# Performance work log

Hardware: AMD Instinct MI355X
Metric: run time of the kernel (lower is better)

## Reference

```python
import jax, jax.numpy as jnp
import numpy as np

B, N, E = 4, 2048, 512
H = 8
HD = E // H  # 64
SCALE = HD ** -0.5


def setup_inputs() -> dict:
    key = jax.random.key(0)
    k1, k2, k3 = jax.random.split(key, 3)
    x = jax.random.normal(k1, (B, N, E), dtype=jnp.float32)
    # xavier-uniform-like scaling for weights
    w_qkv = jax.random.normal(k2, (3 * E, E), dtype=jnp.float32) * (2.0 / (4 * E)) ** 0.5
    b_qkv = jnp.zeros((3 * E,), dtype=jnp.float32)
    w_out = jax.random.normal(k3, (E, E), dtype=jnp.float32) * (1.0 / E) ** 0.5
    b_out = jnp.zeros((E,), dtype=jnp.float32)
    return {"x": x, "w_qkv": w_qkv, "b_qkv": b_qkv, "w_out": w_out, "b_out": b_out}


def reference(x, w_qkv, b_qkv, w_out, b_out):
    b_sz, n_patches, _ = x.shape
    # qkv projection: [B,N,3E] -> [B,N,3,H,HD] -> [B,H,3,N,HD]
    qkv = (jnp.einsum('bne,fe->bnf', x, w_qkv) + b_qkv)
    qkv = qkv.reshape(b_sz, n_patches, 3, H, HD).transpose(0, 3, 2, 1, 4)
    q, k, v = qkv[:, :, 0], qkv[:, :, 1], qkv[:, :, 2]  # each [B,H,N,HD]
    attn = jnp.einsum('bhqd,bhkd->bhqk', q * SCALE, k)  # [B,H,N,N]
    attn = jax.nn.softmax(attn, axis=-1)
    # attn_dropout p=0.0 -> identity in reference
    out = jnp.einsum('bhqk,bhkd->bhqd', attn, v)  # [B,H,N,HD]
    out = out.transpose(0, 2, 1, 3).reshape(b_sz, n_patches, E)
    out = jnp.einsum('bne,fe->bnf', out, w_out) + b_out
    return out
```

## Files before the change

kernel.cpp:

```cpp
#include <hip/hip_runtime.h>

#define BB   4
#define SEQ  2048
#define EMB  512
#define NH   8
#define HD   64
#define QSCALE 0.18033688011f

typedef __bf16 bf16x8 __attribute__((ext_vector_type(8)));
typedef float  f32x4  __attribute__((ext_vector_type(4)));

__device__ __forceinline__ short f2bf(float f) {
  union { float f; unsigned u; } v; v.f = f;
  unsigned r = v.u + 0x7fffu + ((v.u >> 16) & 1u);
  return (short)(r >> 16);
}

__device__ __forceinline__ unsigned pk_bf16(float a, float b) {
#if __has_builtin(__builtin_amdgcn_cvt_pk_bf16_f32)
  typedef __bf16 bf16v2 __attribute__((ext_vector_type(2)));
  union { bf16v2 v; unsigned u; } cv;
  cv.v = __builtin_amdgcn_cvt_pk_bf16_f32(a, b);
  return cv.u;
#else
  return (unsigned)(unsigned short)f2bf(a) | ((unsigned)(unsigned short)f2bf(b) << 16);
#endif
}

__device__ __forceinline__ float fexp2(float x) {
#if __has_builtin(__builtin_amdgcn_exp2f)
  return __builtin_amdgcn_exp2f(x);
#else
  return exp2f(x);
#endif
}

__device__ __forceinline__ void gl_lds16(const void* g, void* l) {
  __builtin_amdgcn_global_load_lds(
      (const __attribute__((address_space(1))) unsigned int*)g,
      (__attribute__((address_space(3))) unsigned int*)l, 16, 0, 0);
}

__global__ __launch_bounds__(256) void cast_all(const float* __restrict__ x,
                                                const float* __restrict__ wq,
                                                const float* __restrict__ wo,
                                                short* __restrict__ xb,
                                                short* __restrict__ wqb,
                                                short* __restrict__ wob) {
  int i = blockIdx.x * 256 + threadIdx.x;
  const float* src; short* dst; int off;
  if (i < 1048576)      { src = x;  dst = xb;  off = i; }
  else if (i < 1245184) { src = wq; dst = wqb; off = i - 1048576; }
  else                  { src = wo; dst = wob; off = i - 1245184; }
  float4 v = ((const float4*)src)[off];
  uint2 o; o.x = pk_bf16(v.x, v.y); o.y = pk_bf16(v.z, v.w);
  *(uint2*)&dst[off * 4] = o;
}

__global__ __launch_bounds__(256) void qkv_gemm(const short* __restrict__ A,
                                                const short* __restrict__ W,
                                                const float* __restrict__ bias,
                                                short* __restrict__ qo,
                                                short* __restrict__ ko,
                                                short* __restrict__ vto) {
  __shared__ __align__(16) short As[128 * 64];
  __shared__ __align__(16) short Bs[128 * 64];
  const int tid  = threadIdx.x;
  const int lane = tid & 63, wave = tid >> 6;
  const int wm = wave >> 1, wf = wave & 1;
  const int col = lane & 15, quad = lane >> 4;
  const int m0 = blockIdx.x * 128, f0 = blockIdx.y * 128;

  const short* aSrc[4]; const short* wSrc[4];
#pragma unroll
  for (int rd = 0; rd < 4; ++rd) {
    int slot = rd * 256 + tid;
    int row = slot >> 3;
    int cb  = (slot & 7) ^ (row & 7);
    aSrc[rd] = A + (size_t)(m0 + row) * 512 + cb * 8;
    wSrc[rd] = W + (size_t)(f0 + row) * 512 + cb * 8;
  }
  int aOff[2][4], bOff[2][4];
#pragma unroll
  for (int kk = 0; kk < 2; ++kk)
#pragma unroll
    for (int i = 0; i < 4; ++i) {
      aOff[kk][i] = (wm * 64 + i * 16 + col) * 64 + (((kk * 4 + quad) ^ (col & 7)) * 8);
      bOff[kk][i] = (wf * 64 + i * 16 + col) * 64 + (((kk * 4 + quad) ^ (col & 7)) * 8);
    }

  f32x4 acc[4][4];
#pragma unroll
  for (int i = 0; i < 4; ++i)
#pragma unroll
    for (int j = 0; j < 4; ++j)
#pragma unroll
      for (int r = 0; r < 4; ++r) acc[i][j][r] = 0.f;

  for (int kt = 0; kt < 8; ++kt) {
    __syncthreads();
#pragma unroll
    for (int rd = 0; rd < 4; ++rd) {
      gl_lds16(aSrc[rd], (char*)As + rd * 4096 + wave * 1024);
      gl_lds16(wSrc[rd], (char*)Bs + rd * 4096 + wave * 1024);
      aSrc[rd] += 64; wSrc[rd] += 64;
    }
    __syncthreads();
#pragma unroll
    for (int kk = 0; kk < 2; ++kk) {
      bf16x8 af[4], bw[4];
#pragma unroll
      for (int i = 0; i < 4; ++i) af[i] = *(const bf16x8*)&As[aOff[kk][i]];
#pragma unroll
      for (int j = 0; j < 4; ++j) bw[j] = *(const bf16x8*)&Bs[bOff[kk][j]];
#pragma unroll
      for (int i = 0; i < 4; ++i)
#pragma unroll
        for (int j = 0; j < 4; ++j)
          acc[i][j] = __builtin_amdgcn_mfma_f32_16x16x32_bf16(af[i], bw[j], acc[i][j], 0, 0, 0);
    }
  }

#pragma unroll
  for (int j = 0; j < 4; ++j) {
    const int f = f0 + wf * 64 + j * 16 + col;
    const float bv = bias[f];
    const int sIdx = f >> 9;
    const int h = (f >> 6) & 7;
    const int d = f & 63;
#pragma unroll
    for (int i = 0; i < 4; ++i) {
      const int mbase = m0 + wm * 64 + i * 16 + quad * 4;
      const int b = mbase >> 11;
      const int n = mbase & 2047;
      const size_t bh = (size_t)(b * NH + h);
      if (sIdx == 2) {
        uint2 pk;
        pk.x = pk_bf16(acc[i][j][0] + bv, acc[i][j][1] + bv);
        pk.y = pk_bf16(acc[i][j][2] + bv, acc[i][j][3] + bv);
        *(uint2*)&vto[(bh * HD + d) * SEQ + n] = pk;
      } else if (sIdx == 0) {
#pragma unroll
        for (int r = 0; r < 4; ++r)
          qo[(bh * SEQ + n + r) * HD + d] = f2bf((acc[i][j][r] + bv) * QSCALE);
      } else {
#pragma unroll
        for (int r = 0; r < 4; ++r)
          ko[(bh * SEQ + n + r) * HD + d] = f2bf(acc[i][j][r] + bv);
      }
    }
  }
}

__global__ __launch_bounds__(256) void attn_kernel(const short* __restrict__ q,
                                                   const short* __restrict__ k,
                                                   const short* __restrict__ vt,
                                                   short* __restrict__ o) {
  __shared__ __align__(16) short Ks[64 * 64];
  __shared__ __align__(16) short Vs[64 * 64];
  __shared__ __align__(16) short Ps[4 * 32 * 72];
  __shared__ float Ls[4 * 32];
  const int tid  = threadIdx.x;
  const int lane = tid & 63, wave = tid >> 6;
  const int col = lane & 15, quad = lane >> 4;
  const int bh = blockIdx.x & 31;
  const int q0 = (blockIdx.x >> 5) * 128;
  const size_t bhBase = (size_t)bh * SEQ * HD;

  bf16x8 qf[2][2];
#pragma unroll
  for (int t = 0; t < 2; ++t)
#pragma unroll
    for (int ks = 0; ks < 2; ++ks)
      qf[t][ks] = *(const bf16x8*)&q[bhBase +
          (size_t)(q0 + wave * 32 + t * 16 + col) * HD + ks * 32 + quad * 8];

  const int rowL = tid >> 3,         cbL = (tid & 7) ^ (rowL & 7);
  const int rowH = (256 + tid) >> 3, cbH = (tid & 7) ^ (rowH & 7);
  const short* ksrcL = k  + bhBase + (size_t)rowL * HD + cbL * 8;
  const short* ksrcH = k  + bhBase + (size_t)rowH * HD + cbH * 8;
  const short* vsrcL = vt + bhBase + (size_t)rowL * SEQ + cbL * 8;
  const short* vsrcH = vt + bhBase + (size_t)rowH * SEQ + cbH * 8;
  char* ldsKL = (char*)Ks + wave * 1024;
  char* ldsKH = (char*)Ks + 4096 + wave * 1024;
  char* ldsVL = (char*)Vs + wave * 1024;
  char* ldsVH = (char*)Vs + 4096 + wave * 1024;

  const int wbase = wave * 32 * 72;
  int kfO[4][2], vfO[2][4], pwO[4][2], prO[2][2];
#pragma unroll
  for (int kt = 0; kt < 4; ++kt)
#pragma unroll
    for (int ks = 0; ks < 2; ++ks)
      kfO[kt][ks] = (kt * 16 + col) * 64 + (((ks * 4 + quad) ^ (col & 7)) * 8);
#pragma unroll
  for (int ks2 = 0; ks2 < 2; ++ks2)
#pragma unroll
    for (int nt = 0; nt < 4; ++nt)
      vfO[ks2][nt] = (nt * 16 + col) * 64 + (((ks2 * 4 + quad) ^ (col & 7)) * 8);
#pragma unroll
  for (int kt = 0; kt < 4; ++kt)
#pragma unroll
    for (int t = 0; t < 2; ++t)
      pwO[kt][t] = wbase + (t * 16 + col) * 72 + kt * 16 + quad * 4;
#pragma unroll
  for (int t = 0; t < 2; ++t)
#pragma unroll
    for (int ks2 = 0; ks2 < 2; ++ks2)
      prO[t][ks2] = wbase + (t * 16 + col) * 72 + ks2 * 32 + quad * 8;

  f32x4 oacc[2][4];
#pragma unroll
  for (int t = 0; t < 2; ++t)
#pragma unroll
    for (int nt = 0; nt < 4; ++nt)
#pragma unroll
      for (int r = 0; r < 4; ++r) oacc[t][nt][r] = 0.f;
  float lpart[2] = {0.f, 0.f};

  for (int n0 = 0; n0 < SEQ; n0 += 64) {
    __syncthreads();
    gl_lds16(ksrcL, ldsKL);
    gl_lds16(ksrcH, ldsKH);
    gl_lds16(vsrcL, ldsVL);
    gl_lds16(vsrcH, ldsVH);
    ksrcL += 64 * HD; ksrcH += 64 * HD; vsrcL += 64; vsrcH += 64;
    __syncthreads();

    f32x4 sacc[4][2];
#pragma unroll
    for (int kt = 0; kt < 4; ++kt)
#pragma unroll
      for (int t = 0; t < 2; ++t)
#pragma unroll
        for (int r = 0; r < 4; ++r) sacc[kt][t][r] = 0.f;
#pragma unroll
    for (int kt = 0; kt < 4; ++kt)
#pragma unroll
      for (int ks = 0; ks < 2; ++ks) {
        bf16x8 kf = *(const bf16x8*)&Ks[kfO[kt][ks]];
#pragma unroll
        for (int t = 0; t < 2; ++t)
          sacc[kt][t] = __builtin_amdgcn_mfma_f32_16x16x32_bf16(kf, qf[t][ks], sacc[kt][t], 0, 0, 0);
      }

#pragma unroll
    for (int kt = 0; kt < 4; ++kt)
#pragma unroll
      for (int t = 0; t < 2; ++t) {
        float p0 = fexp2(sacc[kt][t][0]);
        float p1 = fexp2(sacc[kt][t][1]);
        float p2 = fexp2(sacc[kt][t][2]);
        float p3 = fexp2(sacc[kt][t][3]);
        lpart[t] += (p0 + p1) + (p2 + p3);
        uint2 w; w.x = pk_bf16(p0, p1); w.y = pk_bf16(p2, p3);
        *(uint2*)&Ps[pwO[kt][t]] = w;
      }

#pragma unroll
    for (int ks2 = 0; ks2 < 2; ++ks2) {
      bf16x8 pf[2];
#pragma unroll
      for (int t = 0; t < 2; ++t) pf[t] = *(const bf16x8*)&Ps[prO[t][ks2]];
#pragma unroll
      for (int nt = 0; nt < 4; ++nt) {
        bf16x8 vf = *(const bf16x8*)&Vs[vfO[ks2][nt]];
#pragma unroll
        for (int t = 0; t < 2; ++t)
          oacc[t][nt] = __builtin_amdgcn_mfma_f32_16x16x32_bf16(pf[t], vf, oacc[t][nt], 0, 0, 0);
      }
    }
  }

#pragma unroll
  for (int t = 0; t < 2; ++t) {
    lpart[t] += __shfl_xor(lpart[t], 16);
    lpart[t] += __shfl_xor(lpart[t], 32);
    Ls[wave * 32 + t * 16 + col] = lpart[t];
  }

  const int b = bh >> 3, h = bh & 7;
#pragma unroll
  for (int t = 0; t < 2; ++t) {
    float rl[4];
#pragma unroll
    for (int r = 0; r < 4; ++r)
      rl[r] = 1.0f / Ls[wave * 32 + t * 16 + quad * 4 + r];
#pragma unroll
    for (int nt = 0; nt < 4; ++nt)
#pragma unroll
      for (int r = 0; r < 4; ++r) {
        const int n = q0 + wave * 32 + t * 16 + quad * 4 + r;
        o[((size_t)(b * SEQ + n)) * EMB + h * HD + nt * 16 + col] = f2bf(oacc[t][nt][r] * rl[r]);
      }
  }
}

__global__ __launch_bounds__(256) void proj_gemm(const short* __restrict__ A,
                                                 const short* __restrict__ W,
                                                 const float* __restrict__ bias,
                                                 float* __restrict__ out) {
  __shared__ __align__(16) short As[64 * 64];
  __shared__ __align__(16) short Bs[128 * 64];
  const int tid  = threadIdx.x;
  const int lane = tid & 63, wave = tid >> 6;
  const int wm = wave >> 1, wf = wave & 1;
  const int col = lane & 15, quad = lane >> 4;
  const int m0 = blockIdx.x * 64, f0 = blockIdx.y * 128;

  const short* aSrc[2]; const short* wSrc[4];
#pragma unroll
  for (int rd = 0; rd < 2; ++rd) {
    int slot = rd * 256 + tid;
    int row = slot >> 3;
    int cb  = (slot & 7) ^ (row & 7);
    aSrc[rd] = A + (size_t)(m0 + row) * 512 + cb * 8;
  }
#pragma unroll
  for (int rd = 0; rd < 4; ++rd) {
    int slot = rd * 256 + tid;
    int row = slot >> 3;
    int cb  = (slot & 7) ^ (row & 7);
    wSrc[rd] = W + (size_t)(f0 + row) * 512 + cb * 8;
  }
  int aOff[2][2], bOff[2][4];
#pragma unroll
  for (int kk = 0; kk < 2; ++kk) {
#pragma unroll
    for (int i = 0; i < 2; ++i)
      aOff[kk][i] = (wm * 32 + i * 16 + col) * 64 + (((kk * 4 + quad) ^ (col & 7)) * 8);
#pragma unroll
    for (int j = 0; j < 4; ++j)
      bOff[kk][j] = (wf * 64 + j * 16 + col) * 64 + (((kk * 4 + quad) ^ (col & 7)) * 8);
  }

  f32x4 acc[2][4];
#pragma unroll
  for (int i = 0; i < 2; ++i)
#pragma unroll
    for (int j = 0; j < 4; ++j)
#pragma unroll
      for (int r = 0; r < 4; ++r) acc[i][j][r] = 0.f;

  for (int kt = 0; kt < 8; ++kt) {
    __syncthreads();
#pragma unroll
    for (int rd = 0; rd < 2; ++rd) {
      gl_lds16(aSrc[rd], (char*)As + rd * 4096 + wave * 1024);
      aSrc[rd] += 64;
    }
#pragma unroll
    for (int rd = 0; rd < 4; ++rd) {
      gl_lds16(wSrc[rd], (char*)Bs + rd * 4096 + wave * 1024);
      wSrc[rd] += 64;
    }
    __syncthreads();
#pragma unroll
    for (int kk = 0; kk < 2; ++kk) {
      bf16x8 af[2], bw[4];
#pragma unroll
      for (int i = 0; i < 2; ++i) af[i] = *(const bf16x8*)&As[aOff[kk][i]];
#pragma unroll
      for (int j = 0; j < 4; ++j) bw[j] = *(const bf16x8*)&Bs[bOff[kk][j]];
#pragma unroll
      for (int i = 0; i < 2; ++i)
#pragma unroll
        for (int j = 0; j < 4; ++j)
          acc[i][j] = __builtin_amdgcn_mfma_f32_16x16x32_bf16(af[i], bw[j], acc[i][j], 0, 0, 0);
    }
  }

#pragma unroll
  for (int j = 0; j < 4; ++j) {
    const int f = f0 + wf * 64 + j * 16 + col;
    const float bv = bias[f];
#pragma unroll
    for (int i = 0; i < 2; ++i) {
      const int mbase = m0 + wm * 32 + i * 16 + quad * 4;
#pragma unroll
      for (int r = 0; r < 4; ++r)
        out[(size_t)(mbase + r) * 512 + f] = acc[i][j][r] + bv;
    }
  }
}

extern "C" void kernel_launch(void* const* d_in, const int* in_sizes, int n_in,
                              void* d_out, int out_size, void* d_ws, size_t ws_size,
                              hipStream_t stream) {
  (void)in_sizes; (void)n_in; (void)out_size; (void)ws_size;
  const float* x     = (const float*)d_in[0];
  const float* w_qkv = (const float*)d_in[1];
  const float* b_qkv = (const float*)d_in[2];
  const float* w_out = (const float*)d_in[3];
  const float* b_out = (const float*)d_in[4];
  float* out = (float*)d_out;

  char* ws = (char*)d_ws;
  short* xb    = (short*)(ws + 0);
  short* wqkvb = (short*)(ws + 8388608);
  short* woutb = (short*)(ws + 9961472);
  short* qb    = (short*)(ws + 10485760);
  short* kb    = (short*)(ws + 18874368);
  short* vtb   = (short*)(ws + 27262976);
  short* ob    = (short*)(ws + 35651584);

  cast_all<<<5120, 256, 0, stream>>>(x, w_qkv, w_out, xb, wqkvb, woutb);
  qkv_gemm<<<dim3(64, 12), 256, 0, stream>>>(xb, wqkvb, b_qkv, qb, kb, vtb);
  attn_kernel<<<512, 256, 0, stream>>>(qb, kb, vtb, ob);
  proj_gemm<<<dim3(128, 4), 256, 0, stream>>>(ob, woutb, b_out, out);
}
```

Before: 169.6 us.

## Double-buffer K/V tiles and use 8 waves of 16 query rows in attention

Attention blocks move from 4 waves with 32 query rows each to 8 waves with 16 rows each, so each thread issues one K and one V async global-to-LDS load per tile. K/V tiles are now double-buffered in LDS, so the next tile loads while the current one is computed, and each step needs one barrier instead of two. The row-sum normalisation now uses wave shuffles instead of an LDS array. The trade-off is half the register reuse of each K/V fragment per wave, and more LDS per block, which may limit how many blocks fit on a CU at once.

```diff
diff --git a/kernel.cpp b/kernel.cpp
--- a/kernel.cpp
+++ b/kernel.cpp
@@ -152,14 +152,16 @@
   }
 }
 
-__global__ __launch_bounds__(256) void attn_kernel(const short* __restrict__ q,
+__global__ __launch_bounds__(512) void attn_kernel(const short* __restrict__ q,
                                                    const short* __restrict__ k,
                                                    const short* __restrict__ vt,
                                                    short* __restrict__ o) {
-  __shared__ __align__(16) short Ks[64 * 64];
-  __shared__ __align__(16) short Vs[64 * 64];
-  __shared__ __align__(16) short Ps[4 * 32 * 72];
-  __shared__ float Ls[4 * 32];
+  __shared__ __align__(16) short Ks0[64 * 64];
+  __shared__ __align__(16) short Vs0[64 * 64];
+  __shared__ __align__(16) short Ks1[64 * 64];
+  __shared__ __align__(16) short Vs1[64 * 64];
+  __shared__ __align__(16) short Ps[8 * 16 * 72];
+
   const int tid  = threadIdx.x;
   const int lane = tid & 63, wave = tid >> 6;
   const int col = lane & 15, quad = lane >> 4;
@@ -167,132 +169,91 @@
   const int q0 = (blockIdx.x >> 5) * 128;
   const size_t bhBase = (size_t)bh * SEQ * HD;
 
-  bf16x8 qf[2][2];
-#pragma unroll
-  for (int t = 0; t < 2; ++t)
+  bf16x8 qf[2];
+#pragma unroll
+  for (int ks = 0; ks < 2; ++ks)
+    qf[ks] = *(const bf16x8*)&q[bhBase +
+        (size_t)(q0 + wave * 16 + col) * HD + ks * 32 + quad * 8];
+
+  const int row = tid >> 3, cb = (tid & 7) ^ (row & 7);
+  const short* ksrc = k  + bhBase + (size_t)row * HD  + cb * 8;
+  const short* vsrc = vt + bhBase + (size_t)row * SEQ + cb * 8;
+  char* const ldsK0 = (char*)Ks0 + wave * 1024;
+  char* const ldsV0 = (char*)Vs0 + wave * 1024;
+  char* const ldsK1 = (char*)Ks1 + wave * 1024;
+  char* const ldsV1 = (char*)Vs1 + wave * 1024;
+
+  const int pBase = wave * 16 * 72 + col * 72;
+
+  f32x4 oacc[4];
+#pragma unroll
+  for (int nt = 0; nt < 4; ++nt)
+#pragma unroll
+    for (int r = 0; r < 4; ++r) oacc[nt][r] = 0.f;
+  float lsum = 0.f;
+
+  auto compute = [&](const short* KB, const short* VB) {
+    f32x4 sacc[4];
+#pragma unroll
+    for (int kt = 0; kt < 4; ++kt)
+#pragma unroll
+      for (int r = 0; r < 4; ++r) sacc[kt][r] = 0.f;
 #pragma unroll
     for (int ks = 0; ks < 2; ++ks)
-      qf[t][ks] = *(const bf16x8*)&q[bhBase +
-          (size_t)(q0 + wave * 32 + t * 16 + col) * HD + ks * 32 + quad * 8];
-
-  const int rowL = tid >> 3,         cbL = (tid & 7) ^ (rowL & 7);
-  const int rowH = (256 + tid) >> 3, cbH = (tid & 7) ^ (rowH & 7);
-  const short* ksrcL = k  + bhBase + (size_t)rowL * HD + cbL * 8;
-  const short* ksrcH = k  + bhBase + (size_t)rowH * HD + cbH * 8;
-  const short* vsrcL = vt + bhBase + (size_t)rowL * SEQ + cbL * 8;
-  const short* vsrcH = vt + bhBase + (size_t)rowH * SEQ + cbH * 8;
-  char* ldsKL = (char*)Ks + wave * 1024;
-  char* ldsKH = (char*)Ks + 4096 + wave * 1024;
-  char* ldsVL = (char*)Vs + wave * 1024;
-  char* ldsVH = (char*)Vs + 4096 + wave * 1024;
-
-  const int wbase = wave * 32 * 72;
-  int kfO[4][2], vfO[2][4], pwO[4][2], prO[2][2];
-#pragma unroll
-  for (int kt = 0; kt < 4; ++kt)
-#pragma unroll
-    for (int ks = 0; ks < 2; ++ks)
-      kfO[kt][ks] = (kt * 16 + col) * 64 + (((ks * 4 + quad) ^ (col & 7)) * 8);
-#pragma unroll
-  for (int ks2 = 0; ks2 < 2; ++ks2)
+#pragma unroll
+      for (int kt = 0; kt < 4; ++kt) {
+        bf16x8 kf = *(const bf16x8*)&KB[(kt * 16 + col) * 64 +
+                                        (((ks * 4 + quad) ^ (col & 7)) * 8)];
+        sacc[kt] = __builtin_amdgcn_mfma_f32_16x16x32_bf16(kf, qf[ks], sacc[kt], 0, 0, 0);
+      }
+#pragma unroll
+    for (int kt = 0; kt < 4; ++kt) {
+      float p0 = fexp2(sacc[kt][0]);
+      float p1 = fexp2(sacc[kt][1]);
+      float p2 = fexp2(sacc[kt][2]);
+      float p3 = fexp2(sacc[kt][3]);
+      lsum += (p0 + p1) + (p2 + p3);
+      uint2 w; w.x = pk_bf16(p0, p1); w.y = pk_bf16(p2, p3);
+      *(uint2*)&Ps[pBase + kt * 16 + quad * 4] = w;
+    }
+#pragma unroll
+    for (int ks2 = 0; ks2 < 2; ++ks2) {
+      bf16x8 pf = *(const bf16x8*)&Ps[pBase + ks2 * 32 + quad * 8];
+#pragma unroll
+      for (int nt = 0; nt < 4; ++nt) {
+        bf16x8 vf = *(const bf16x8*)&VB[(nt * 16 + col) * 64 +
+                                        (((ks2 * 4 + quad) ^ (col & 7)) * 8)];
+        oacc[nt] = __builtin_amdgcn_mfma_f32_16x16x32_bf16(pf, vf, oacc[nt], 0, 0, 0);
+      }
+    }
+  };
+
+  gl_lds16(ksrc, ldsK0); gl_lds16(vsrc, ldsV0);
+  ksrc += 64 * HD; vsrc += 64;
+  __syncthreads();
+
+  for (int t = 0; t < 32; t += 2) {
+    gl_lds16(ksrc, ldsK1); gl_lds16(vsrc, ldsV1);
+    ksrc += 64 * HD; vsrc += 64;
+    compute(Ks0, Vs0);
+    __syncthreads();
+    gl_lds16(ksrc, ldsK0); gl_lds16(vsrc, ldsV0);
+    ksrc += 64 * HD; vsrc += 64;
+    compute(Ks1, Vs1);
+    __syncthreads();
+  }
+
+  lsum += __shfl_xor(lsum, 16);
+  lsum += __shfl_xor(lsum, 32);
+
+  const int b = bh >> 3, h = bh & 7;
+#pragma unroll
+  for (int r = 0; r < 4; ++r) {
+    const float rl = 1.0f / __shfl(lsum, quad * 4 + r);
+    const int n = q0 + wave * 16 + quad * 4 + r;
 #pragma unroll
     for (int nt = 0; nt < 4; ++nt)
-      vfO[ks2][nt] = (nt * 16 + col) * 64 + (((ks2 * 4 + quad) ^ (col & 7)) * 8);
-#pragma unroll
-  for (int kt = 0; kt < 4; ++kt)
-#pragma unroll
-    for (int t = 0; t < 2; ++t)
-      pwO[kt][t] = wbase + (t * 16 + col) * 72 + kt * 16 + quad * 4;
-#pragma unroll
-  for (int t = 0; t < 2; ++t)
-#pragma unroll
-    for (int ks2 = 0; ks2 < 2; ++ks2)
-      prO[t][ks2] = wbase + (t * 16 + col) * 72 + ks2 * 32 + quad * 8;
-
-  f32x4 oacc[2][4];
-#pragma unroll
-  for (int t = 0; t < 2; ++t)
-#pragma unroll
-    for (int nt = 0; nt < 4; ++nt)
-#pragma unroll
-      for (int r = 0; r < 4; ++r) oacc[t][nt][r] = 0.f;
-  float lpart[2] = {0.f, 0.f};
-
-  for (int n0 = 0; n0 < SEQ; n0 += 64) {
-    __syncthreads();
-    gl_lds16(ksrcL, ldsKL);
-    gl_lds16(ksrcH, ldsKH);
-    gl_lds16(vsrcL, ldsVL);
-    gl_lds16(vsrcH, ldsVH);
-    ksrcL += 64 * HD; ksrcH += 64 * HD; vsrcL += 64; vsrcH += 64;
-    __syncthreads();
-
-    f32x4 sacc[4][2];
-#pragma unroll
-    for (int kt = 0; kt < 4; ++kt)
-#pragma unroll
-      for (int t = 0; t < 2; ++t)
-#pragma unroll
-        for (int r = 0; r < 4; ++r) sacc[kt][t][r] = 0.f;
-#pragma unroll
-    for (int kt = 0; kt < 4; ++kt)
-#pragma unroll
-      for (int ks = 0; ks < 2; ++ks) {
-        bf16x8 kf = *(const bf16x8*)&Ks[kfO[kt][ks]];
-#pragma unroll
-        for (int t = 0; t < 2; ++t)
-          sacc[kt][t] = __builtin_amdgcn_mfma_f32_16x16x32_bf16(kf, qf[t][ks], sacc[kt][t], 0, 0, 0);
-      }
-
-#pragma unroll
-    for (int kt = 0; kt < 4; ++kt)
-#pragma unroll
-      for (int t = 0; t < 2; ++t) {
-        float p0 = fexp2(sacc[kt][t][0]);
-        float p1 = fexp2(sacc[kt][t][1]);
-        float p2 = fexp2(sacc[kt][t][2]);
-        float p3 = fexp2(sacc[kt][t][3]);
-        lpart[t] += (p0 + p1) + (p2 + p3);
-        uint2 w; w.x = pk_bf16(p0, p1); w.y = pk_bf16(p2, p3);
-        *(uint2*)&Ps[pwO[kt][t]] = w;
-      }
-
-#pragma unroll
-    for (int ks2 = 0; ks2 < 2; ++ks2) {
-      bf16x8 pf[2];
-#pragma unroll
-      for (int t = 0; t < 2; ++t) pf[t] = *(const bf16x8*)&Ps[prO[t][ks2]];
-#pragma unroll
-      for (int nt = 0; nt < 4; ++nt) {
-        bf16x8 vf = *(const bf16x8*)&Vs[vfO[ks2][nt]];
-#pragma unroll
-        for (int t = 0; t < 2; ++t)
-          oacc[t][nt] = __builtin_amdgcn_mfma_f32_16x16x32_bf16(pf[t], vf, oacc[t][nt], 0, 0, 0);
-      }
-    }
-  }
-
-#pragma unroll
-  for (int t = 0; t < 2; ++t) {
-    lpart[t] += __shfl_xor(lpart[t], 16);
-    lpart[t] += __shfl_xor(lpart[t], 32);
-    Ls[wave * 32 + t * 16 + col] = lpart[t];
-  }
-
-  const int b = bh >> 3, h = bh & 7;
-#pragma unroll
-  for (int t = 0; t < 2; ++t) {
-    float rl[4];
-#pragma unroll
-    for (int r = 0; r < 4; ++r)
-      rl[r] = 1.0f / Ls[wave * 32 + t * 16 + quad * 4 + r];
-#pragma unroll
-    for (int nt = 0; nt < 4; ++nt)
-#pragma unroll
-      for (int r = 0; r < 4; ++r) {
-        const int n = q0 + wave * 32 + t * 16 + quad * 4 + r;
-        o[((size_t)(b * SEQ + n)) * EMB + h * HD + nt * 16 + col] = f2bf(oacc[t][nt][r] * rl[r]);
-      }
+      o[((size_t)(b * SEQ + n)) * EMB + h * HD + nt * 16 + col] = f2bf(oacc[nt][r] * rl);
   }
 }
 
@@ -406,6 +367,6 @@
 
   cast_all<<<5120, 256, 0, stream>>>(x, w_qkv, w_out, xb, wqkvb, woutb);
   qkv_gemm<<<dim3(64, 12), 256, 0, stream>>>(xb, wqkvb, b_qkv, qb, kb, vtb);
-  attn_kernel<<<512, 256, 0, stream>>>(qb, kb, vtb, ob);
+  attn_kernel<<<512, 512, 0, stream>>>(qb, kb, vtb, ob);
   proj_gemm<<<dim3(128, 4), 256, 0, stream>>>(ob, woutb, b_out, out);
 }
```

New measurement: 160.8 us. 5.2% less time.

## Double-buffer K/V tiles in LDS to overlap loads with attention compute

Applied to the files above, without the earlier changes.

Adds a second set of K and V LDS buffers. The kernel now prefetches the next 64-key tile through the async global-to-LDS path while it computes on the current tile, and needs one barrier per tile instead of two. The aim is to hide global load latency behind the MFMA and exp work. In exchange, LDS use per block roughly doubles for K/V, which may lower occupancy. The final iteration also prefetches one tile past the end of the sequence, an out-of-range read whose data is never used.

```diff
diff --git a/kernel.cpp b/kernel.cpp
--- a/kernel.cpp
+++ b/kernel.cpp
@@ -156,10 +156,13 @@
                                                    const short* __restrict__ k,
                                                    const short* __restrict__ vt,
                                                    short* __restrict__ o) {
-  __shared__ __align__(16) short Ks[64 * 64];
-  __shared__ __align__(16) short Vs[64 * 64];
+  __shared__ __align__(16) short Ks0[64 * 64];
+  __shared__ __align__(16) short Vs0[64 * 64];
+  __shared__ __align__(16) short Ks1[64 * 64];
+  __shared__ __align__(16) short Vs1[64 * 64];
   __shared__ __align__(16) short Ps[4 * 32 * 72];
   __shared__ float Ls[4 * 32];
+
   const int tid  = threadIdx.x;
   const int lane = tid & 63, wave = tid >> 6;
   const int col = lane & 15, quad = lane >> 4;
@@ -181,10 +184,14 @@
   const short* ksrcH = k  + bhBase + (size_t)rowH * HD + cbH * 8;
   const short* vsrcL = vt + bhBase + (size_t)rowL * SEQ + cbL * 8;
   const short* vsrcH = vt + bhBase + (size_t)rowH * SEQ + cbH * 8;
-  char* ldsKL = (char*)Ks + wave * 1024;
-  char* ldsKH = (char*)Ks + 4096 + wave * 1024;
-  char* ldsVL = (char*)Vs + wave * 1024;
-  char* ldsVH = (char*)Vs + 4096 + wave * 1024;
+  char* const ldsK0L = (char*)Ks0 + wave * 1024;
+  char* const ldsK0H = (char*)Ks0 + 4096 + wave * 1024;
+  char* const ldsV0L = (char*)Vs0 + wave * 1024;
+  char* const ldsV0H = (char*)Vs0 + 4096 + wave * 1024;
+  char* const ldsK1L = (char*)Ks1 + wave * 1024;
+  char* const ldsK1H = (char*)Ks1 + 4096 + wave * 1024;
+  char* const ldsV1L = (char*)Vs1 + wave * 1024;
+  char* const ldsV1H = (char*)Vs1 + 4096 + wave * 1024;
 
   const int wbase = wave * 32 * 72;
   int kfO[4][2], vfO[2][4], pwO[4][2], prO[2][2];
@@ -218,15 +225,7 @@
       for (int r = 0; r < 4; ++r) oacc[t][nt][r] = 0.f;
   float lpart[2] = {0.f, 0.f};
 
-  for (int n0 = 0; n0 < SEQ; n0 += 64) {
-    __syncthreads();
-    gl_lds16(ksrcL, ldsKL);
-    gl_lds16(ksrcH, ldsKH);
-    gl_lds16(vsrcL, ldsVL);
-    gl_lds16(vsrcH, ldsVH);
-    ksrcL += 64 * HD; ksrcH += 64 * HD; vsrcL += 64; vsrcH += 64;
-    __syncthreads();
-
+  auto compute = [&](const short* KB, const short* VB) {
     f32x4 sacc[4][2];
 #pragma unroll
     for (int kt = 0; kt < 4; ++kt)
@@ -238,7 +237,7 @@
     for (int kt = 0; kt < 4; ++kt)
 #pragma unroll
       for (int ks = 0; ks < 2; ++ks) {
-        bf16x8 kf = *(const bf16x8*)&Ks[kfO[kt][ks]];
+        bf16x8 kf = *(const bf16x8*)&KB[kfO[kt][ks]];
 #pragma unroll
         for (int t = 0; t < 2; ++t)
           sacc[kt][t] = __builtin_amdgcn_mfma_f32_16x16x32_bf16(kf, qf[t][ks], sacc[kt][t], 0, 0, 0);
@@ -264,12 +263,30 @@
       for (int t = 0; t < 2; ++t) pf[t] = *(const bf16x8*)&Ps[prO[t][ks2]];
 #pragma unroll
       for (int nt = 0; nt < 4; ++nt) {
-        bf16x8 vf = *(const bf16x8*)&Vs[vfO[ks2][nt]];
+        bf16x8 vf = *(const bf16x8*)&VB[vfO[ks2][nt]];
 #pragma unroll
         for (int t = 0; t < 2; ++t)
           oacc[t][nt] = __builtin_amdgcn_mfma_f32_16x16x32_bf16(pf[t], vf, oacc[t][nt], 0, 0, 0);
       }
     }
+  };
+
+  gl_lds16(ksrcL, ldsK0L); gl_lds16(ksrcH, ldsK0H);
+  gl_lds16(vsrcL, ldsV0L); gl_lds16(vsrcH, ldsV0H);
+  ksrcL += 64 * HD; ksrcH += 64 * HD; vsrcL += 64; vsrcH += 64;
+  __syncthreads();
+
+  for (int t = 0; t < 32; t += 2) {
+    gl_lds16(ksrcL, ldsK1L); gl_lds16(ksrcH, ldsK1H);
+    gl_lds16(vsrcL, ldsV1L); gl_lds16(vsrcH, ldsV1H);
+    ksrcL += 64 * HD; ksrcH += 64 * HD; vsrcL += 64; vsrcH += 64;
+    compute(Ks0, Vs0);
+    __syncthreads();
+    gl_lds16(ksrcL, ldsK0L); gl_lds16(ksrcH, ldsK0H);
+    gl_lds16(vsrcL, ldsV0L); gl_lds16(vsrcH, ldsV0H);
+    ksrcL += 64 * HD; ksrcH += 64 * HD; vsrcL += 64; vsrcH += 64;
+    compute(Ks1, Vs1);
+    __syncthreads();
   }
 
 #pragma unroll
```

Result: no change. 169.0 us (-0.3%).
